# Optimization experiments

Measured on AMD Instinct MI355X. Metric: run time of the kernel, lower is better.

## Reference

```python
import jax, jax.numpy as jnp
import numpy as np

N_VOX, N_COLS = 200000, 5   # (N, 1 + 3 coords + 1 feat)
N_CLUSTS, PTS_PER_CLUST = 1024, 128
N_EDGES = 8192


def setup_inputs() -> dict:
    key = jax.random.key(0)
    k1, k2, k3 = jax.random.split(key, 3)
    data = jax.random.normal(k1, (N_VOX, N_COLS), dtype=jnp.float32)
    clusts = jax.random.randint(k2, (N_CLUSTS, PTS_PER_CLUST), 0, N_VOX)
    edge_index = jax.random.randint(k3, (2, N_EDGES), 0, N_CLUSTS)
    return {"data": data, "clusts": clusts, "edge_index": edge_index}


def reference(data, clusts, edge_index):
    # COORD_COLS = columns 1:4 of the sparse tensor
    voxels = data[:, 1:4]                       # [N, 3]
    pts = voxels[clusts]                        # [C, P, 3]
    x1 = pts[edge_index[0]]                     # [E, P, 3] first cluster of each edge
    x2 = pts[edge_index[1]]                     # [E, P, 3] second cluster
    P = x1.shape[1]

    # per-edge pairwise squared distances (argmin of d^2 == argmin of d)
    d2 = jnp.sum((x1[:, :, None, :] - x2[:, None, :, :]) ** 2, axis=-1)  # [E, P, P]
    imin = jnp.argmin(d2.reshape(d2.shape[0], -1), axis=1)               # [E]
    i1, i2 = imin // P, imin % P

    v1 = jnp.take_along_axis(x1, i1[:, None, None], axis=1)[:, 0, :]     # [E, 3]
    v2 = jnp.take_along_axis(x2, i2[:, None, None], axis=1)[:, 0, :]     # [E, 3]

    disp = v1 - v2
    lend = jnp.linalg.norm(disp, axis=-1, keepdims=True)                 # [E, 1]
    safe = jnp.where(lend > 0, lend, 1.0)
    dispn = jnp.where(lend > 0, disp / safe, disp)                       # unit displacement

    B = (dispn[:, :, None] * dispn[:, None, :]).reshape(-1, 9)           # outer product, [E, 9]

    feats = jnp.concatenate([v1, v2, dispn, lend, B], axis=1)            # [E, 19]
    # undirected: interleave original and flipped (v1<->v2, disp -> -disp, B invariant)
    feats_flip = jnp.concatenate([v2, v1, -dispn, lend, B], axis=1)
    full = jnp.stack([feats, feats_flip], axis=1).reshape(-1, 19)        # [2E, 19]
    return full
```

## Files before the change

### kernel.cpp

```cpp
#include <hip/hip_runtime.h>
#include <cstdint>

#define NV 200000
#define NCOLS 5
#define P 128
#define NE 8192
#define NC 1024

__global__ __launch_bounds__(256) void gather_kernel(
    const float* __restrict__ data,
    const int*   __restrict__ clusts,
    float4*      __restrict__ ws)
{
    const int idx = blockIdx.x * 256 + threadIdx.x;
    const int v = clusts[idx];
    ws[idx] = make_float4(data[v * NCOLS + 1], data[v * NCOLS + 2],
                          data[v * NCOLS + 3], 0.f);
}

template <bool USE_WS>
__global__ __launch_bounds__(256) void clust_geo_edge_kernel(
    const float*  __restrict__ data,
    const int*    __restrict__ clusts,
    const int*    __restrict__ edge_index,
    const float4* __restrict__ ws,
    float*        __restrict__ out)
{
    const int e = blockIdx.x;
    const int t = threadIdx.x;

    __shared__ float4 x1s[P];
    __shared__ float4 x2s[P];
    __shared__ unsigned long long wmin[4];

    const int c1 = edge_index[e];
    const int c2 = edge_index[NE + e];

    if (USE_WS) {
        if (t < P) x1s[t]     = ws[c1 * P + t];
        else       x2s[t - P] = ws[c2 * P + (t - P)];
    } else {
        if (t < P) {
            const int v = clusts[c1 * P + t];
            x1s[t] = make_float4(data[v * NCOLS + 1], data[v * NCOLS + 2],
                                 data[v * NCOLS + 3], 0.f);
        } else {
            const int p = t - P;
            const int v = clusts[c2 * P + p];
            x2s[p] = make_float4(data[v * NCOLS + 1], data[v * NCOLS + 2],
                                 data[v * NCOLS + 3], 0.f);
        }
    }
    __syncthreads();

    const int tj = t & 15;
    const int ti = t >> 4;

    float4 a[8], b[8];
    #pragma unroll
    for (int k = 0; k < 8; ++k) a[k] = x1s[ti + 16 * k];
    #pragma unroll
    for (int m = 0; m < 8; ++m) b[m] = x2s[tj + 16 * m];

    float bd[8];
    int   bj[8];
    #pragma unroll
    for (int k = 0; k < 8; ++k) { bd[k] = __builtin_inff(); bj[k] = 0; }

    #pragma unroll
    for (int m = 0; m < 8; ++m) {
        const int j = tj + 16 * m;
        const float bx = b[m].x, by = b[m].y, bz = b[m].z;
        #pragma unroll
        for (int k = 0; k < 8; ++k) {
            const float dx = __fsub_rn(a[k].x, bx);
            const float dy = __fsub_rn(a[k].y, by);
            const float dz = __fsub_rn(a[k].z, bz);
            const float d2 = __fadd_rn(__fadd_rn(__fmul_rn(dx, dx), __fmul_rn(dy, dy)),
                                       __fmul_rn(dz, dz));
            if (d2 < bd[k]) { bd[k] = d2; bj[k] = j; }
        }
    }

    float bestd = __builtin_inff();
    int   bestflat = 0;
    #pragma unroll
    for (int k = 0; k < 8; ++k) {
        if (bd[k] < bestd) { bestd = bd[k]; bestflat = (ti + 16 * k) * P + bj[k]; }
    }

    unsigned long long key =
        ((unsigned long long)__float_as_uint(bestd) << 32) | (unsigned)bestflat;

    for (int off = 32; off > 0; off >>= 1) {
        unsigned long long other = __shfl_down(key, off, 64);
        if (other < key) key = other;
    }
    const int wave = t >> 6;
    if ((t & 63) == 0) wmin[wave] = key;
    __syncthreads();

    if (t == 0) {
        unsigned long long k0 = wmin[0];
        #pragma unroll
        for (int w = 1; w < 4; ++w) if (wmin[w] < k0) k0 = wmin[w];
        const int flat = (int)(k0 & 0xffffffffull);
        const int i1 = flat >> 7;
        const int i2 = flat & (P - 1);

        const float v1x = x1s[i1].x, v1y = x1s[i1].y, v1z = x1s[i1].z;
        const float v2x = x2s[i2].x, v2y = x2s[i2].y, v2z = x2s[i2].z;

        const float dx = v1x - v2x, dy = v1y - v2y, dz = v1z - v2z;
        const float lend = sqrtf(dx * dx + dy * dy + dz * dz);

        float nx, ny, nz;
        if (lend > 0.f) { nx = dx / lend; ny = dy / lend; nz = dz / lend; }
        else            { nx = dx;        ny = dy;        nz = dz;        }

        const float B[9] = { nx*nx, nx*ny, nx*nz,
                             ny*nx, ny*ny, ny*nz,
                             nz*nx, nz*ny, nz*nz };

        float* o = out + (size_t)e * 38;
        o[0] = v1x; o[1] = v1y; o[2] = v1z;
        o[3] = v2x; o[4] = v2y; o[5] = v2z;
        o[6] = nx;  o[7] = ny;  o[8] = nz;  o[9] = lend;
        #pragma unroll
        for (int q = 0; q < 9; ++q) o[10 + q] = B[q];
        o[19] = v2x; o[20] = v2y; o[21] = v2z;
        o[22] = v1x; o[23] = v1y; o[24] = v1z;
        o[25] = -nx; o[26] = -ny; o[27] = -nz; o[28] = lend;
        #pragma unroll
        for (int q = 0; q < 9; ++q) o[29 + q] = B[q];
    }
}

extern "C" void kernel_launch(void* const* d_in, const int* in_sizes, int n_in,
                              void* d_out, int out_size, void* d_ws, size_t ws_size,
                              hipStream_t stream) {
    const float* data       = (const float*)d_in[0];
    const int*   clusts     = (const int*)d_in[1];
    const int*   edge_index = (const int*)d_in[2];
    float*       out        = (float*)d_out;
    float4*      ws         = (float4*)d_ws;

    const size_t need = (size_t)NC * P * sizeof(float4);
    if (ws_size >= need) {
        gather_kernel<<<(NC * P) / 256, 256, 0, stream>>>(data, clusts, ws);
        clust_geo_edge_kernel<true><<<NE, 256, 0, stream>>>(data, clusts, edge_index, ws, out);
    } else {
        clust_geo_edge_kernel<false><<<NE, 256, 0, stream>>>(data, clusts, edge_index, ws, out);
    }
}
```

Measured before the change: 95.00 us.

## Map one wavefront per edge, two edges per block, drop cross-wave reduction

Reassigns the work so each 64-lane wavefront handles a whole edge, and a 128-thread block packs two edges. This removes the shared-memory cross-wave argmin reduction and the second barrier. The inner loop is restructured to keep a running min per row, cutting register arrays. Each lane now does four times more distance evaluations, so latency per edge grows while block-level sync overhead falls.

```diff
diff --git a/kernel.cpp b/kernel.cpp
--- a/kernel.cpp
+++ b/kernel.cpp
@@ -19,74 +19,75 @@
 }
 
 template <bool USE_WS>
-__global__ __launch_bounds__(256) void clust_geo_edge_kernel(
+__global__ __launch_bounds__(128) void clust_geo_edge_kernel(
     const float*  __restrict__ data,
     const int*    __restrict__ clusts,
     const int*    __restrict__ edge_index,
     const float4* __restrict__ ws,
     float*        __restrict__ out)
 {
-    const int e = blockIdx.x;
-    const int t = threadIdx.x;
+    const int w    = threadIdx.x >> 6;
+    const int lane = threadIdx.x & 63;
+    const int e    = blockIdx.x * 2 + w;
 
-    __shared__ float4 x1s[P];
-    __shared__ float4 x2s[P];
-    __shared__ unsigned long long wmin[4];
+    __shared__ float4 x1s[2][P];
+    __shared__ float4 x2s[2][P];
 
     const int c1 = edge_index[e];
     const int c2 = edge_index[NE + e];
 
     if (USE_WS) {
-        if (t < P) x1s[t]     = ws[c1 * P + t];
-        else       x2s[t - P] = ws[c2 * P + (t - P)];
+        x1s[w][lane]      = ws[c1 * P + lane];
+        x1s[w][lane + 64] = ws[c1 * P + lane + 64];
+        x2s[w][lane]      = ws[c2 * P + lane];
+        x2s[w][lane + 64] = ws[c2 * P + lane + 64];
     } else {
-        if (t < P) {
-            const int v = clusts[c1 * P + t];
-            x1s[t] = make_float4(data[v * NCOLS + 1], data[v * NCOLS + 2],
-                                 data[v * NCOLS + 3], 0.f);
-        } else {
-            const int p = t - P;
-            const int v = clusts[c2 * P + p];
-            x2s[p] = make_float4(data[v * NCOLS + 1], data[v * NCOLS + 2],
-                                 data[v * NCOLS + 3], 0.f);
-        }
+        int v = clusts[c1 * P + lane];
+        x1s[w][lane]      = make_float4(data[v * NCOLS + 1], data[v * NCOLS + 2],
+                                        data[v * NCOLS + 3], 0.f);
+        v = clusts[c1 * P + lane + 64];
+        x1s[w][lane + 64] = make_float4(data[v * NCOLS + 1], data[v * NCOLS + 2],
+                                        data[v * NCOLS + 3], 0.f);
+        v = clusts[c2 * P + lane];
+        x2s[w][lane]      = make_float4(data[v * NCOLS + 1], data[v * NCOLS + 2],
+                                        data[v * NCOLS + 3], 0.f);
+        v = clusts[c2 * P + lane + 64];
+        x2s[w][lane + 64] = make_float4(data[v * NCOLS + 1], data[v * NCOLS + 2],
+                                        data[v * NCOLS + 3], 0.f);
     }
     __syncthreads();
 
-    const int tj = t & 15;
-    const int ti = t >> 4;
+    const int tj = lane & 15;
+    const int ti = lane >> 4;
 
-    float4 a[8], b[8];
+    float bx[8], by[8], bz[8];
     #pragma unroll
-    for (int k = 0; k < 8; ++k) a[k] = x1s[ti + 16 * k];
-    #pragma unroll
-    for (int m = 0; m < 8; ++m) b[m] = x2s[tj + 16 * m];
+    for (int m = 0; m < 8; ++m) {
+        const float4 v = x2s[w][tj + 16 * m];
+        bx[m] = v.x; by[m] = v.y; bz[m] = v.z;
+    }
 
-    float bd[8];
-    int   bj[8];
-    #pragma unroll
-    for (int k = 0; k < 8; ++k) { bd[k] = __builtin_inff(); bj[k] = 0; }
+    float bestd    = __builtin_inff();
+    int   bestflat = 0;
 
     #pragma unroll
-    for (int m = 0; m < 8; ++m) {
-        const int j = tj + 16 * m;
-        const float bx = b[m].x, by = b[m].y, bz = b[m].z;
+    for (int k = 0; k < 32; ++k) {
+        const int i = ti + 4 * k;
+        const float4 av = x1s[w][i];
+        const float ax = av.x, ay = av.y, az = av.z;
+
+        float dmin = __builtin_inff();
+        int   bj   = 0;
         #pragma unroll
-        for (int k = 0; k < 8; ++k) {
-            const float dx = __fsub_rn(a[k].x, bx);
-            const float dy = __fsub_rn(a[k].y, by);
-            const float dz = __fsub_rn(a[k].z, bz);
+        for (int m = 0; m < 8; ++m) {
+            const float dx = __fsub_rn(ax, bx[m]);
+            const float dy = __fsub_rn(ay, by[m]);
+            const float dz = __fsub_rn(az, bz[m]);
             const float d2 = __fadd_rn(__fadd_rn(__fmul_rn(dx, dx), __fmul_rn(dy, dy)),
                                        __fmul_rn(dz, dz));
-            if (d2 < bd[k]) { bd[k] = d2; bj[k] = j; }
+            if (d2 < dmin) { dmin = d2; bj = tj + 16 * m; }
         }
-    }
-
-    float bestd = __builtin_inff();
-    int   bestflat = 0;
-    #pragma unroll
-    for (int k = 0; k < 8; ++k) {
-        if (bd[k] < bestd) { bestd = bd[k]; bestflat = (ti + 16 * k) * P + bj[k]; }
+        if (dmin < bestd) { bestd = dmin; bestflat = i * P + bj; }
     }
 
     unsigned long long key =
@@ -96,20 +97,14 @@
         unsigned long long other = __shfl_down(key, off, 64);
         if (other < key) key = other;
     }
-    const int wave = t >> 6;
-    if ((t & 63) == 0) wmin[wave] = key;
-    __syncthreads();
 
-    if (t == 0) {
-        unsigned long long k0 = wmin[0];
-        #pragma unroll
-        for (int w = 1; w < 4; ++w) if (wmin[w] < k0) k0 = wmin[w];
-        const int flat = (int)(k0 & 0xffffffffull);
+    if (lane == 0) {
+        const int flat = (int)(key & 0xffffffffull);
         const int i1 = flat >> 7;
         const int i2 = flat & (P - 1);
 
-        const float v1x = x1s[i1].x, v1y = x1s[i1].y, v1z = x1s[i1].z;
-        const float v2x = x2s[i2].x, v2y = x2s[i2].y, v2z = x2s[i2].z;
+        const float v1x = x1s[w][i1].x, v1y = x1s[w][i1].y, v1z = x1s[w][i1].z;
+        const float v2x = x2s[w][i2].x, v2y = x2s[w][i2].y, v2z = x2s[w][i2].z;
 
         const float dx = v1x - v2x, dy = v1y - v2y, dz = v1z - v2z;
         const float lend = sqrtf(dx * dx + dy * dy + dz * dz);
@@ -148,8 +143,8 @@
     const size_t need = (size_t)NC * P * sizeof(float4);
     if (ws_size >= need) {
         gather_kernel<<<(NC * P) / 256, 256, 0, stream>>>(data, clusts, ws);
-        clust_geo_edge_kernel<true><<<NE, 256, 0, stream>>>(data, clusts, edge_index, ws, out);
+        clust_geo_edge_kernel<true><<<NE / 2, 128, 0, stream>>>(data, clusts, edge_index, ws, out);
     } else {
-        clust_geo_edge_kernel<false><<<NE, 256, 0, stream>>>(data, clusts, edge_index, ws, out);
+        clust_geo_edge_kernel<false><<<NE / 2, 128, 0, stream>>>(data, clusts, edge_index, ws, out);
     }
 }
```

New measurement: 96.26 us. About the same (+1.3%).
